# Kernel optimization log

Measured on AMD Instinct MI355X. Metric: run time of the kernel, lower is better.

The kernel has to match this reference:

```python
import jax, jax.numpy as jnp
import numpy as np

N = 262144
H = 256
R = 32


def setup_inputs() -> dict:
    key = jax.random.key(0)
    ks = jax.random.split(key, 16)
    s = 1.0 / np.sqrt(H)
    return {
        "x": jax.random.normal(ks[0], (N, 1), jnp.float32),
        "t": jax.random.uniform(ks[1], (N, 1), jnp.float32),
        "start_w": jax.random.normal(ks[2], (H, 2), jnp.float32) * 0.5,
        "start_b": jax.random.normal(ks[3], (H,), jnp.float32) * 0.1,
        "end_w": jax.random.normal(ks[4], (1, H), jnp.float32) * s,
        "end_b": jax.random.normal(ks[5], (1,), jnp.float32) * 0.1,
        "col_0": jax.random.normal(ks[6], (H, R), jnp.float32) * s,
        "col_1": jax.random.normal(ks[7], (H, R), jnp.float32) * s,
        "col_2": jax.random.normal(ks[8], (H, R), jnp.float32) * s,
        "row_0": jax.random.normal(ks[9], (H, R), jnp.float32) * s,
        "row_1": jax.random.normal(ks[10], (H, R), jnp.float32) * s,
        "row_2": jax.random.normal(ks[11], (H, R), jnp.float32) * s,
        "alpha_0": jax.random.normal(ks[12], (R,), jnp.float32),
        "alpha_1": jax.random.normal(ks[13], (R,), jnp.float32),
        "alpha_2": jax.random.normal(ks[14], (R,), jnp.float32),
    }


def reference(x, t, start_w, start_b, end_w, end_b,
              col_0, col_1, col_2, row_0, row_1, row_2,
              alpha_0, alpha_1, alpha_2):
    # inputs: [N,2] -> start Linear -> tanh
    inp = jnp.concatenate([x, t], axis=1)
    h = jnp.tanh(inp @ start_w.T + start_b)  # [N, H]
    # three low-rank blocks: h @ (col * diag(alpha)) @ row.T, then tanh.
    # col_basis @ diag(alpha) == col_basis * alpha[None, :] (column scaling)
    for col, row, alpha in ((col_0, row_0, alpha_0),
                            (col_1, row_1, alpha_1),
                            (col_2, row_2, alpha_2)):
        h = jnp.tanh((h @ (col * alpha)) @ row.T)  # [N,H]->[N,R]->[N,H]
    return h @ end_w.T + end_b  # [N, 1]
```

## Files before the change

kernel.cpp:

```cpp
#include <hip/hip_runtime.h>


typedef _Float16 half4_t __attribute__((ext_vector_type(4)));
typedef float    float4_t __attribute__((ext_vector_type(4)));

namespace {

struct Smem {
  half4_t ctf[3 * 16 * 2 * 64];
  half4_t rwf[3 * 16 * 2 * 64];
  float w0[256], w1[256], bb[256], ew[256];
};

__device__ __forceinline__ float fast_tanh(float x) {
  float e = __builtin_amdgcn_exp2f(x * 2.885390081777927f);
  return 1.0f - 2.0f * __builtin_amdgcn_rcpf(e + 1.0f);
}

__device__ __forceinline__ half4_t tanh4_pack(float4_t v) {
  half4_t h;
  h.x = (_Float16)fast_tanh(v.x);
  h.y = (_Float16)fast_tanh(v.y);
  h.z = (_Float16)fast_tanh(v.z);
  h.w = (_Float16)fast_tanh(v.w);
  return h;
}

__device__ __forceinline__ half4_t pack16(float4_t v) {
  half4_t h;
  h.x = (_Float16)v.x; h.y = (_Float16)v.y; h.z = (_Float16)v.z; h.w = (_Float16)v.w;
  return h;
}

__global__ __launch_bounds__(1024)
__attribute__((amdgpu_waves_per_eu(4, 4)))
void pinn_fused(
    const float* __restrict__ xg, const float* __restrict__ tg,
    const float* __restrict__ sw, const float* __restrict__ sb,
    const float* __restrict__ ewp, const float* __restrict__ ebp,
    const float* __restrict__ c0, const float* __restrict__ c1,
    const float* __restrict__ c2, const float* __restrict__ r0,
    const float* __restrict__ r1, const float* __restrict__ r2,
    const float* __restrict__ a0, const float* __restrict__ a1,
    const float* __restrict__ a2, float* __restrict__ out, int n)
{
  __shared__ Smem sm;
  const int tid = threadIdx.x;

  for (int e = tid; e < 3 * 16 * 2 * 64; e += 1024) {
    const int lane_ = e & 63;
    const int sel   = (e >> 6) & 1;
    const int t_    = (e >> 7) & 15;
    const int k_    = e >> 11;
    const int m_ = lane_ & 15, q_ = lane_ >> 4;
    const float* ck = (k_ == 0) ? c0 : (k_ == 1) ? c1 : c2;
    const float* rk = (k_ == 0) ? r0 : (k_ == 1) ? r1 : r2;
    const float* ak = (k_ == 0) ? a0 : (k_ == 1) ? a1 : a2;
    {
      const int r = sel * 16 + m_;
      const float av = ak[r];
      const int j0 = 16 * t_ + 4 * q_;
      half4_t v;
      v.x = (_Float16)(ck[(j0 + 0) * 32 + r] * av);
      v.y = (_Float16)(ck[(j0 + 1) * 32 + r] * av);
      v.z = (_Float16)(ck[(j0 + 2) * 32 + r] * av);
      v.w = (_Float16)(ck[(j0 + 3) * 32 + r] * av);
      sm.ctf[e] = v;
    }
    {
      const int j = 16 * t_ + m_;
      const int rr = sel * 16 + 4 * q_;
      half4_t v;
      v.x = (_Float16)rk[j * 32 + rr + 0];
      v.y = (_Float16)rk[j * 32 + rr + 1];
      v.z = (_Float16)rk[j * 32 + rr + 2];
      v.w = (_Float16)rk[j * 32 + rr + 3];
      sm.rwf[e] = v;
    }
  }
  if (tid < 256) {
    sm.w0[tid] = sw[2 * tid];
    sm.w1[tid] = sw[2 * tid + 1];
    sm.bb[tid] = sb[tid];
    sm.ew[tid] = ewp[tid];
  }
  __syncthreads();

  const int wave = tid >> 6;
  const int lane = tid & 63;
  const int m = lane & 15;
  const int q = lane >> 4;
  const int wo = 4 * q;
  const float ebv = ebp[0];
  const int tiles = n >> 4;

#pragma unroll 1
  for (int g = blockIdx.x * 32 + wave * 2; g < tiles; g += 8192) {
    const int n0 = g * 16;
    const int n1 = n0 + 16;
    const float xm0 = xg[n0 + m], tm0 = tg[n0 + m];
    const float xm1 = xg[n1 + m], tm1 = tg[n1 + m];

    float4_t a00 = {0.f, 0.f, 0.f, 0.f}, a01 = {0.f, 0.f, 0.f, 0.f};
    float4_t a10 = {0.f, 0.f, 0.f, 0.f}, a11 = {0.f, 0.f, 0.f, 0.f};
#pragma unroll 1
    for (int t = 0; t < 16; ++t) {
      const int cb = t * 16 + wo;
      const float4_t w0v = *(const float4_t*)&sm.w0[cb];
      const float4_t w1v = *(const float4_t*)&sm.w1[cb];
      const float4_t bv  = *(const float4_t*)&sm.bb[cb];
      float4_t z0, z1;
      z0.x = fmaf(xm0, w0v.x, fmaf(tm0, w1v.x, bv.x));
      z0.y = fmaf(xm0, w0v.y, fmaf(tm0, w1v.y, bv.y));
      z0.z = fmaf(xm0, w0v.z, fmaf(tm0, w1v.z, bv.z));
      z0.w = fmaf(xm0, w0v.w, fmaf(tm0, w1v.w, bv.w));
      z1.x = fmaf(xm1, w0v.x, fmaf(tm1, w1v.x, bv.x));
      z1.y = fmaf(xm1, w0v.y, fmaf(tm1, w1v.y, bv.y));
      z1.z = fmaf(xm1, w0v.z, fmaf(tm1, w1v.z, bv.z));
      z1.w = fmaf(xm1, w0v.w, fmaf(tm1, w1v.w, bv.w));
      const half4_t h0 = tanh4_pack(z0);
      const half4_t h1 = tanh4_pack(z1);
      const half4_t cA = sm.ctf[t * 128 + lane];
      const half4_t cB = sm.ctf[t * 128 + 64 + lane];
      a00 = __builtin_amdgcn_mfma_f32_16x16x16f16(cA, h0, a00, 0, 0, 0);
      a01 = __builtin_amdgcn_mfma_f32_16x16x16f16(cB, h0, a01, 0, 0, 0);
      a10 = __builtin_amdgcn_mfma_f32_16x16x16f16(cA, h1, a10, 0, 0, 0);
      a11 = __builtin_amdgcn_mfma_f32_16x16x16f16(cB, h1, a11, 0, 0, 0);
    }

    float ssum0 = 0.0f, ssum1 = 0.0f;
#pragma unroll 1
    for (int k = 0; k < 3; ++k) {
      const half4_t pA0 = pack16(a00), pB0 = pack16(a01);
      const half4_t pA1 = pack16(a10), pB1 = pack16(a11);

      if (k < 2) {
        float4_t n00 = {0.f, 0.f, 0.f, 0.f}, n01 = {0.f, 0.f, 0.f, 0.f};
        float4_t n10 = {0.f, 0.f, 0.f, 0.f}, n11 = {0.f, 0.f, 0.f, 0.f};
        const half4_t* rp = &sm.rwf[k * 2048 + lane];
        const half4_t* cp = &sm.ctf[(k + 1) * 2048 + lane];
#pragma unroll 1
        for (int t = 0; t < 16; ++t) {
          const half4_t rA = rp[0], rB = rp[64];
          const half4_t cA = cp[0], cB = cp[64];
          float4_t hc0 = {0.f, 0.f, 0.f, 0.f};
          hc0 = __builtin_amdgcn_mfma_f32_16x16x16f16(rA, pA0, hc0, 0, 0, 0);
          hc0 = __builtin_amdgcn_mfma_f32_16x16x16f16(rB, pB0, hc0, 0, 0, 0);
          float4_t hc1 = {0.f, 0.f, 0.f, 0.f};
          hc1 = __builtin_amdgcn_mfma_f32_16x16x16f16(rA, pA1, hc1, 0, 0, 0);
          hc1 = __builtin_amdgcn_mfma_f32_16x16x16f16(rB, pB1, hc1, 0, 0, 0);
          const half4_t h0 = tanh4_pack(hc0);
          const half4_t h1 = tanh4_pack(hc1);
          n00 = __builtin_amdgcn_mfma_f32_16x16x16f16(cA, h0, n00, 0, 0, 0);
          n01 = __builtin_amdgcn_mfma_f32_16x16x16f16(cB, h0, n01, 0, 0, 0);
          n10 = __builtin_amdgcn_mfma_f32_16x16x16f16(cA, h1, n10, 0, 0, 0);
          n11 = __builtin_amdgcn_mfma_f32_16x16x16f16(cB, h1, n11, 0, 0, 0);
          rp += 128;
          cp += 128;
        }
        a00 = n00; a01 = n01; a10 = n10; a11 = n11;
      } else {
        const half4_t* rp = &sm.rwf[2 * 2048 + lane];
#pragma unroll 1
        for (int t = 0; t < 16; ++t) {
          const half4_t rA = rp[0], rB = rp[64];
          float4_t hc0 = {0.f, 0.f, 0.f, 0.f};
          hc0 = __builtin_amdgcn_mfma_f32_16x16x16f16(rA, pA0, hc0, 0, 0, 0);
          hc0 = __builtin_amdgcn_mfma_f32_16x16x16f16(rB, pB0, hc0, 0, 0, 0);
          float4_t hc1 = {0.f, 0.f, 0.f, 0.f};
          hc1 = __builtin_amdgcn_mfma_f32_16x16x16f16(rA, pA1, hc1, 0, 0, 0);
          hc1 = __builtin_amdgcn_mfma_f32_16x16x16f16(rB, pB1, hc1, 0, 0, 0);
          const float4_t ev = *(const float4_t*)&sm.ew[t * 16 + wo];
          ssum0 += fast_tanh(hc0.x) * ev.x + fast_tanh(hc0.y) * ev.y
                 + fast_tanh(hc0.z) * ev.z + fast_tanh(hc0.w) * ev.w;
          ssum1 += fast_tanh(hc1.x) * ev.x + fast_tanh(hc1.y) * ev.y
                 + fast_tanh(hc1.z) * ev.z + fast_tanh(hc1.w) * ev.w;
          rp += 128;
        }
      }
    }
    ssum0 += __shfl_xor(ssum0, 16);
    ssum0 += __shfl_xor(ssum0, 32);
    ssum1 += __shfl_xor(ssum1, 16);
    ssum1 += __shfl_xor(ssum1, 32);
    if (lane < 16) {
      out[n0 + m] = ssum0 + ebv;
      out[n1 + m] = ssum1 + ebv;
    }
  }
}

}

extern "C" void kernel_launch(void* const* d_in, const int* in_sizes, int n_in,
                              void* d_out, int out_size, void* d_ws, size_t ws_size,
                              hipStream_t stream) {
  const float* xg  = (const float*)d_in[0];
  const float* tg  = (const float*)d_in[1];
  const float* sw  = (const float*)d_in[2];
  const float* sb  = (const float*)d_in[3];
  const float* ewp = (const float*)d_in[4];
  const float* ebp = (const float*)d_in[5];
  const float* c0  = (const float*)d_in[6];
  const float* c1  = (const float*)d_in[7];
  const float* c2  = (const float*)d_in[8];
  const float* r0  = (const float*)d_in[9];
  const float* r1  = (const float*)d_in[10];
  const float* r2  = (const float*)d_in[11];
  const float* a0  = (const float*)d_in[12];
  const float* a1  = (const float*)d_in[13];
  const float* a2  = (const float*)d_in[14];
  float* outp = (float*)d_out;

  const int n = in_sizes[0];

  pinn_fused<<<256, 1024, 0, stream>>>(xg, tg, sw, sb, ewp, ebp,
                                       c0, c1, c2, r0, r1, r2, a0, a1, a2,
                                       outp, n);
}
```

Baseline: 153.8 us.

## Fold tanh affine parts into weights and batch reciprocals across eight values

After: 160.2 us. 4.1% more time.

```diff
diff --git a/kernel.cpp b/kernel.cpp
--- a/kernel.cpp
+++ b/kernel.cpp
@@ -4,26 +4,37 @@
 typedef _Float16 half4_t __attribute__((ext_vector_type(4)));
 typedef float    float4_t __attribute__((ext_vector_type(4)));
 
+#define TANH_SCALE 2.885390081777927f
+#define ECLAMP 32768.0f
+
 namespace {
 
-struct Smem {
+struct alignas(16) Smem {
   half4_t ctf[3 * 16 * 2 * 64];
   half4_t rwf[3 * 16 * 2 * 64];
-  float w0[256], w1[256], bb[256], ew[256];
+  float w0[256], w1[256], bb[256];
+  float ew[256];
+  float rsC[3 * 32];
 };
 
-__device__ __forceinline__ float fast_tanh(float x) {
-  float e = __builtin_amdgcn_exp2f(x * 2.885390081777927f);
-  return 1.0f - 2.0f * __builtin_amdgcn_rcpf(e + 1.0f);
-}
-
-__device__ __forceinline__ half4_t tanh4_pack(float4_t v) {
-  half4_t h;
-  h.x = (_Float16)fast_tanh(v.x);
-  h.y = (_Float16)fast_tanh(v.y);
-  h.z = (_Float16)fast_tanh(v.z);
-  h.w = (_Float16)fast_tanh(v.w);
-  return h;
+__device__ __forceinline__ void inv8(float4_t v0, float4_t v1,
+                                     float4_t& i0, float4_t& i1) {
+  const float a0 = fminf(__builtin_amdgcn_exp2f(v0.x), ECLAMP) + 1.0f;
+  const float a1 = fminf(__builtin_amdgcn_exp2f(v0.y), ECLAMP) + 1.0f;
+  const float a2 = fminf(__builtin_amdgcn_exp2f(v0.z), ECLAMP) + 1.0f;
+  const float a3 = fminf(__builtin_amdgcn_exp2f(v0.w), ECLAMP) + 1.0f;
+  const float a4 = fminf(__builtin_amdgcn_exp2f(v1.x), ECLAMP) + 1.0f;
+  const float a5 = fminf(__builtin_amdgcn_exp2f(v1.y), ECLAMP) + 1.0f;
+  const float a6 = fminf(__builtin_amdgcn_exp2f(v1.z), ECLAMP) + 1.0f;
+  const float a7 = fminf(__builtin_amdgcn_exp2f(v1.w), ECLAMP) + 1.0f;
+  const float p01 = a0 * a1, p23 = a2 * a3, p45 = a4 * a5, p67 = a6 * a7;
+  const float q03 = p01 * p23, q47 = p45 * p67;
+  const float rd = __builtin_amdgcn_rcpf(q03 * q47);
+  const float s03 = rd * q47, s47 = rd * q03;
+  const float t01 = s03 * p23, t23 = s03 * p01;
+  const float t45 = s47 * p67, t67 = s47 * p45;
+  i0.x = t01 * a1; i0.y = t01 * a0; i0.z = t23 * a3; i0.w = t23 * a2;
+  i1.x = t45 * a5; i1.y = t45 * a4; i1.z = t67 * a7; i1.w = t67 * a6;
 }
 
 __device__ __forceinline__ half4_t pack16(float4_t v) {
@@ -58,7 +69,7 @@
     const float* ak = (k_ == 0) ? a0 : (k_ == 1) ? a1 : a2;
     {
       const int r = sel * 16 + m_;
-      const float av = ak[r];
+      const float av = ak[r] * -2.0f;
       const int j0 = 16 * t_ + 4 * q_;
       half4_t v;
       v.x = (_Float16)(ck[(j0 + 0) * 32 + r] * av);
@@ -71,18 +82,31 @@
       const int j = 16 * t_ + m_;
       const int rr = sel * 16 + 4 * q_;
       half4_t v;
-      v.x = (_Float16)rk[j * 32 + rr + 0];
-      v.y = (_Float16)rk[j * 32 + rr + 1];
-      v.z = (_Float16)rk[j * 32 + rr + 2];
-      v.w = (_Float16)rk[j * 32 + rr + 3];
+      v.x = (_Float16)(rk[j * 32 + rr + 0] * TANH_SCALE);
+      v.y = (_Float16)(rk[j * 32 + rr + 1] * TANH_SCALE);
+      v.z = (_Float16)(rk[j * 32 + rr + 2] * TANH_SCALE);
+      v.w = (_Float16)(rk[j * 32 + rr + 3] * TANH_SCALE);
       sm.rwf[e] = v;
     }
   }
   if (tid < 256) {
-    sm.w0[tid] = sw[2 * tid];
-    sm.w1[tid] = sw[2 * tid + 1];
-    sm.bb[tid] = sb[tid];
-    sm.ew[tid] = ewp[tid];
+    sm.w0[tid] = sw[2 * tid] * TANH_SCALE;
+    sm.w1[tid] = sw[2 * tid + 1] * TANH_SCALE;
+    sm.bb[tid] = sb[tid] * TANH_SCALE;
+    sm.ew[tid] = ewp[tid] * -2.0f;
+  }
+  __syncthreads();
+
+  if (tid < 96) {
+    const int k_ = tid >> 5, r = tid & 31;
+    const int sel = r >> 4, mm = r & 15;
+    float s = 0.0f;
+    for (int t = 0; t < 16; ++t)
+      for (int qq = 0; qq < 4; ++qq) {
+        const half4_t v = sm.ctf[((k_ * 16 + t) * 2 + sel) * 64 + 16 * qq + mm];
+        s += (float)v.x + (float)v.y + (float)v.z + (float)v.w;
+      }
+    sm.rsC[k_ * 32 + r] = -0.5f * s;
   }
   __syncthreads();
 
@@ -94,6 +118,13 @@
   const float ebv = ebp[0];
   const int tiles = n >> 4;
 
+  float ewsum = 0.0f;
+  for (int t = 0; t < 16; ++t) {
+    const float4_t e4 = *(const float4_t*)&sm.ew[t * 16 + wo];
+    ewsum += e4.x + e4.y + e4.z + e4.w;
+  }
+  ewsum *= -0.5f;
+
 #pragma unroll 1
   for (int g = blockIdx.x * 32 + wave * 2; g < tiles; g += 8192) {
     const int n0 = g * 16;
@@ -101,8 +132,10 @@
     const float xm0 = xg[n0 + m], tm0 = tg[n0 + m];
     const float xm1 = xg[n1 + m], tm1 = tg[n1 + m];
 
-    float4_t a00 = {0.f, 0.f, 0.f, 0.f}, a01 = {0.f, 0.f, 0.f, 0.f};
-    float4_t a10 = {0.f, 0.f, 0.f, 0.f}, a11 = {0.f, 0.f, 0.f, 0.f};
+    const float4_t rs00 = *(const float4_t*)&sm.rsC[0 * 32 + wo];
+    const float4_t rs01 = *(const float4_t*)&sm.rsC[0 * 32 + 16 + wo];
+    float4_t a00 = rs00, a01 = rs01;
+    float4_t a10 = rs00, a11 = rs01;
 #pragma unroll 1
     for (int t = 0; t < 16; ++t) {
       const int cb = t * 16 + wo;
@@ -111,32 +144,35 @@
       const float4_t bv  = *(const float4_t*)&sm.bb[cb];
       float4_t z0, z1;
       z0.x = fmaf(xm0, w0v.x, fmaf(tm0, w1v.x, bv.x));
+      z1.x = fmaf(xm1, w0v.x, fmaf(tm1, w1v.x, bv.x));
       z0.y = fmaf(xm0, w0v.y, fmaf(tm0, w1v.y, bv.y));
+      z1.y = fmaf(xm1, w0v.y, fmaf(tm1, w1v.y, bv.y));
       z0.z = fmaf(xm0, w0v.z, fmaf(tm0, w1v.z, bv.z));
+      z1.z = fmaf(xm1, w0v.z, fmaf(tm1, w1v.z, bv.z));
       z0.w = fmaf(xm0, w0v.w, fmaf(tm0, w1v.w, bv.w));
-      z1.x = fmaf(xm1, w0v.x, fmaf(tm1, w1v.x, bv.x));
-      z1.y = fmaf(xm1, w0v.y, fmaf(tm1, w1v.y, bv.y));
-      z1.z = fmaf(xm1, w0v.z, fmaf(tm1, w1v.z, bv.z));
       z1.w = fmaf(xm1, w0v.w, fmaf(tm1, w1v.w, bv.w));
-      const half4_t h0 = tanh4_pack(z0);
-      const half4_t h1 = tanh4_pack(z1);
+      float4_t i0, i1;
+      inv8(z0, z1, i0, i1);
+      const half4_t h0 = pack16(i0);
+      const half4_t h1 = pack16(i1);
       const half4_t cA = sm.ctf[t * 128 + lane];
       const half4_t cB = sm.ctf[t * 128 + 64 + lane];
       a00 = __builtin_amdgcn_mfma_f32_16x16x16f16(cA, h0, a00, 0, 0, 0);
+      a10 = __builtin_amdgcn_mfma_f32_16x16x16f16(cA, h1, a10, 0, 0, 0);
       a01 = __builtin_amdgcn_mfma_f32_16x16x16f16(cB, h0, a01, 0, 0, 0);
-      a10 = __builtin_amdgcn_mfma_f32_16x16x16f16(cA, h1, a10, 0, 0, 0);
       a11 = __builtin_amdgcn_mfma_f32_16x16x16f16(cB, h1, a11, 0, 0, 0);
     }
 
-    float ssum0 = 0.0f, ssum1 = 0.0f;
+    float ssum0 = ewsum, ssum1 = ewsum;
 #pragma unroll 1
     for (int k = 0; k < 3; ++k) {
       const half4_t pA0 = pack16(a00), pB0 = pack16(a01);
       const half4_t pA1 = pack16(a10), pB1 = pack16(a11);
 
       if (k < 2) {
-        float4_t n00 = {0.f, 0.f, 0.f, 0.f}, n01 = {0.f, 0.f, 0.f, 0.f};
-        float4_t n10 = {0.f, 0.f, 0.f, 0.f}, n11 = {0.f, 0.f, 0.f, 0.f};
+        const float4_t rsA = *(const float4_t*)&sm.rsC[(k + 1) * 32 + wo];
+        const float4_t rsB = *(const float4_t*)&sm.rsC[(k + 1) * 32 + 16 + wo];
+        float4_t n00 = rsA, n01 = rsB, n10 = rsA, n11 = rsB;
         const half4_t* rp = &sm.rwf[k * 2048 + lane];
         const half4_t* cp = &sm.ctf[(k + 1) * 2048 + lane];
 #pragma unroll 1
@@ -144,16 +180,18 @@
           const half4_t rA = rp[0], rB = rp[64];
           const half4_t cA = cp[0], cB = cp[64];
           float4_t hc0 = {0.f, 0.f, 0.f, 0.f};
+          float4_t hc1 = {0.f, 0.f, 0.f, 0.f};
           hc0 = __builtin_amdgcn_mfma_f32_16x16x16f16(rA, pA0, hc0, 0, 0, 0);
+          hc1 = __builtin_amdgcn_mfma_f32_16x16x16f16(rA, pA1, hc1, 0, 0, 0);
           hc0 = __builtin_amdgcn_mfma_f32_16x16x16f16(rB, pB0, hc0, 0, 0, 0);
-          float4_t hc1 = {0.f, 0.f, 0.f, 0.f};
-          hc1 = __builtin_amdgcn_mfma_f32_16x16x16f16(rA, pA1, hc1, 0, 0, 0);
           hc1 = __builtin_amdgcn_mfma_f32_16x16x16f16(rB, pB1, hc1, 0, 0, 0);
-          const half4_t h0 = tanh4_pack(hc0);
-          const half4_t h1 = tanh4_pack(hc1);
+          float4_t i0, i1;
+          inv8(hc0, hc1, i0, i1);
+          const half4_t h0 = pack16(i0);
+          const half4_t h1 = pack16(i1);
           n00 = __builtin_amdgcn_mfma_f32_16x16x16f16(cA, h0, n00, 0, 0, 0);
+          n10 = __builtin_amdgcn_mfma_f32_16x16x16f16(cA, h1, n10, 0, 0, 0);
           n01 = __builtin_amdgcn_mfma_f32_16x16x16f16(cB, h0, n01, 0, 0, 0);
-          n10 = __builtin_amdgcn_mfma_f32_16x16x16f16(cA, h1, n10, 0, 0, 0);
           n11 = __builtin_amdgcn_mfma_f32_16x16x16f16(cB, h1, n11, 0, 0, 0);
           rp += 128;
           cp += 128;
@@ -165,16 +203,16 @@
         for (int t = 0; t < 16; ++t) {
           const half4_t rA = rp[0], rB = rp[64];
           float4_t hc0 = {0.f, 0.f, 0.f, 0.f};
+          float4_t hc1 = {0.f, 0.f, 0.f, 0.f};
           hc0 = __builtin_amdgcn_mfma_f32_16x16x16f16(rA, pA0, hc0, 0, 0, 0);
+          hc1 = __builtin_amdgcn_mfma_f32_16x16x16f16(rA, pA1, hc1, 0, 0, 0);
           hc0 = __builtin_amdgcn_mfma_f32_16x16x16f16(rB, pB0, hc0, 0, 0, 0);
-          float4_t hc1 = {0.f, 0.f, 0.f, 0.f};
-          hc1 = __builtin_amdgcn_mfma_f32_16x16x16f16(rA, pA1, hc1, 0, 0, 0);
           hc1 = __builtin_amdgcn_mfma_f32_16x16x16f16(rB, pB1, hc1, 0, 0, 0);
+          float4_t i0, i1;
+          inv8(hc0, hc1, i0, i1);
           const float4_t ev = *(const float4_t*)&sm.ew[t * 16 + wo];
-          ssum0 += fast_tanh(hc0.x) * ev.x + fast_tanh(hc0.y) * ev.y
-                 + fast_tanh(hc0.z) * ev.z + fast_tanh(hc0.w) * ev.w;
-          ssum1 += fast_tanh(hc1.x) * ev.x + fast_tanh(hc1.y) * ev.y
-                 + fast_tanh(hc1.z) * ev.z + fast_tanh(hc1.w) * ev.w;
+          ssum0 += ev.x * i0.x + ev.y * i0.y + ev.z * i0.z + ev.w * i0.w;
+          ssum1 += ev.x * i1.x + ev.y * i1.y + ev.z * i1.z + ev.w * i1.w;
           rp += 128;
         }
       }
```

## Software-pipeline MFMA/tanh loops and fold tanh scale into weights

Applied to the files above, without the earlier changes.

Result: faster. 150.1 us (-2.4%).

```diff
diff --git a/kernel.cpp b/kernel.cpp
--- a/kernel.cpp
+++ b/kernel.cpp
@@ -2,34 +2,39 @@
 
 
 typedef _Float16 half4_t __attribute__((ext_vector_type(4)));
+typedef _Float16 half2_t __attribute__((ext_vector_type(2)));
+typedef __fp16   fp16x2  __attribute__((ext_vector_type(2)));
 typedef float    float4_t __attribute__((ext_vector_type(4)));
 
+#define TANH_SCALE 2.885390081777927f
+#define MFMA16 __builtin_amdgcn_mfma_f32_16x16x16f16
+
 namespace {
 
-struct Smem {
+struct alignas(16) Smem {
   half4_t ctf[3 * 16 * 2 * 64];
   half4_t rwf[3 * 16 * 2 * 64];
-  float w0[256], w1[256], bb[256], ew[256];
+  float w0[256], w1[256], bb[256];
+  float ew[256];
 };
 
-__device__ __forceinline__ float fast_tanh(float x) {
-  float e = __builtin_amdgcn_exp2f(x * 2.885390081777927f);
-  return 1.0f - 2.0f * __builtin_amdgcn_rcpf(e + 1.0f);
-}
-
-__device__ __forceinline__ half4_t tanh4_pack(float4_t v) {
-  half4_t h;
-  h.x = (_Float16)fast_tanh(v.x);
-  h.y = (_Float16)fast_tanh(v.y);
-  h.z = (_Float16)fast_tanh(v.z);
-  h.w = (_Float16)fast_tanh(v.w);
-  return h;
-}
-
-__device__ __forceinline__ half4_t pack16(float4_t v) {
-  half4_t h;
-  h.x = (_Float16)v.x; h.y = (_Float16)v.y; h.z = (_Float16)v.z; h.w = (_Float16)v.w;
-  return h;
+__device__ __forceinline__ half4_t pack4(float4_t v) {
+  union { fp16x2 f2[2]; half4_t h4; } u;
+  u.f2[0] = __builtin_amdgcn_cvt_pkrtz(v.x, v.y);
+  u.f2[1] = __builtin_amdgcn_cvt_pkrtz(v.z, v.w);
+  return u.h4;
+}
+
+__device__ __forceinline__ float tanh_pre(float y) {
+  const float e = __builtin_amdgcn_exp2f(y);
+  return fmaf(-2.0f, __builtin_amdgcn_rcpf(e + 1.0f), 1.0f);
+}
+
+__device__ __forceinline__ half4_t tanh4(float4_t v) {
+  float4_t r;
+  r.x = tanh_pre(v.x); r.y = tanh_pre(v.y);
+  r.z = tanh_pre(v.z); r.w = tanh_pre(v.w);
+  return pack4(r);
 }
 
 __global__ __launch_bounds__(1024)
@@ -71,17 +76,17 @@
       const int j = 16 * t_ + m_;
       const int rr = sel * 16 + 4 * q_;
       half4_t v;
-      v.x = (_Float16)rk[j * 32 + rr + 0];
-      v.y = (_Float16)rk[j * 32 + rr + 1];
-      v.z = (_Float16)rk[j * 32 + rr + 2];
-      v.w = (_Float16)rk[j * 32 + rr + 3];
+      v.x = (_Float16)(rk[j * 32 + rr + 0] * TANH_SCALE);
+      v.y = (_Float16)(rk[j * 32 + rr + 1] * TANH_SCALE);
+      v.z = (_Float16)(rk[j * 32 + rr + 2] * TANH_SCALE);
+      v.w = (_Float16)(rk[j * 32 + rr + 3] * TANH_SCALE);
       sm.rwf[e] = v;
     }
   }
   if (tid < 256) {
-    sm.w0[tid] = sw[2 * tid];
-    sm.w1[tid] = sw[2 * tid + 1];
-    sm.bb[tid] = sb[tid];
+    sm.w0[tid] = sw[2 * tid] * TANH_SCALE;
+    sm.w1[tid] = sw[2 * tid + 1] * TANH_SCALE;
+    sm.bb[tid] = sb[tid] * TANH_SCALE;
     sm.ew[tid] = ewp[tid];
   }
   __syncthreads();
@@ -94,6 +99,8 @@
   const float ebv = ebp[0];
   const int tiles = n >> 4;
 
+  const float4_t z4 = {0.f, 0.f, 0.f, 0.f};
+
 #pragma unroll 1
   for (int g = blockIdx.x * 32 + wave * 2; g < tiles; g += 8192) {
     const int n0 = g * 16;
@@ -101,84 +108,146 @@
     const float xm0 = xg[n0 + m], tm0 = tg[n0 + m];
     const float xm1 = xg[n1 + m], tm1 = tg[n1 + m];
 
-    float4_t a00 = {0.f, 0.f, 0.f, 0.f}, a01 = {0.f, 0.f, 0.f, 0.f};
-    float4_t a10 = {0.f, 0.f, 0.f, 0.f}, a11 = {0.f, 0.f, 0.f, 0.f};
-#pragma unroll 1
-    for (int t = 0; t < 16; ++t) {
-      const int cb = t * 16 + wo;
+    float4_t a00 = z4, a01 = z4, a10 = z4, a11 = z4;
+    float4_t zc0, zc1;
+    {
+      const float4_t w0v = *(const float4_t*)&sm.w0[wo];
+      const float4_t w1v = *(const float4_t*)&sm.w1[wo];
+      const float4_t bv  = *(const float4_t*)&sm.bb[wo];
+      zc0.x = fmaf(xm0, w0v.x, fmaf(tm0, w1v.x, bv.x));
+      zc1.x = fmaf(xm1, w0v.x, fmaf(tm1, w1v.x, bv.x));
+      zc0.y = fmaf(xm0, w0v.y, fmaf(tm0, w1v.y, bv.y));
+      zc1.y = fmaf(xm1, w0v.y, fmaf(tm1, w1v.y, bv.y));
+      zc0.z = fmaf(xm0, w0v.z, fmaf(tm0, w1v.z, bv.z));
+      zc1.z = fmaf(xm1, w0v.z, fmaf(tm1, w1v.z, bv.z));
+      zc0.w = fmaf(xm0, w0v.w, fmaf(tm0, w1v.w, bv.w));
+      zc1.w = fmaf(xm1, w0v.w, fmaf(tm1, w1v.w, bv.w));
+    }
+    const half4_t* cp0 = &sm.ctf[lane];
+#pragma unroll 1
+    for (int t = 0; t < 15; ++t) {
+      const int cb = (t + 1) * 16 + wo;
       const float4_t w0v = *(const float4_t*)&sm.w0[cb];
       const float4_t w1v = *(const float4_t*)&sm.w1[cb];
       const float4_t bv  = *(const float4_t*)&sm.bb[cb];
-      float4_t z0, z1;
-      z0.x = fmaf(xm0, w0v.x, fmaf(tm0, w1v.x, bv.x));
-      z0.y = fmaf(xm0, w0v.y, fmaf(tm0, w1v.y, bv.y));
-      z0.z = fmaf(xm0, w0v.z, fmaf(tm0, w1v.z, bv.z));
-      z0.w = fmaf(xm0, w0v.w, fmaf(tm0, w1v.w, bv.w));
-      z1.x = fmaf(xm1, w0v.x, fmaf(tm1, w1v.x, bv.x));
-      z1.y = fmaf(xm1, w0v.y, fmaf(tm1, w1v.y, bv.y));
-      z1.z = fmaf(xm1, w0v.z, fmaf(tm1, w1v.z, bv.z));
-      z1.w = fmaf(xm1, w0v.w, fmaf(tm1, w1v.w, bv.w));
-      const half4_t h0 = tanh4_pack(z0);
-      const half4_t h1 = tanh4_pack(z1);
-      const half4_t cA = sm.ctf[t * 128 + lane];
-      const half4_t cB = sm.ctf[t * 128 + 64 + lane];
-      a00 = __builtin_amdgcn_mfma_f32_16x16x16f16(cA, h0, a00, 0, 0, 0);
-      a01 = __builtin_amdgcn_mfma_f32_16x16x16f16(cB, h0, a01, 0, 0, 0);
-      a10 = __builtin_amdgcn_mfma_f32_16x16x16f16(cA, h1, a10, 0, 0, 0);
-      a11 = __builtin_amdgcn_mfma_f32_16x16x16f16(cB, h1, a11, 0, 0, 0);
+      const half4_t h0 = tanh4(zc0);
+      const half4_t h1 = tanh4(zc1);
+      float4_t zn0, zn1;
+      zn0.x = fmaf(xm0, w0v.x, fmaf(tm0, w1v.x, bv.x));
+      zn1.x = fmaf(xm1, w0v.x, fmaf(tm1, w1v.x, bv.x));
+      zn0.y = fmaf(xm0, w0v.y, fmaf(tm0, w1v.y, bv.y));
+      zn1.y = fmaf(xm1, w0v.y, fmaf(tm1, w1v.y, bv.y));
+      zn0.z = fmaf(xm0, w0v.z, fmaf(tm0, w1v.z, bv.z));
+      zn1.z = fmaf(xm1, w0v.z, fmaf(tm1, w1v.z, bv.z));
+      zn0.w = fmaf(xm0, w0v.w, fmaf(tm0, w1v.w, bv.w));
+      zn1.w = fmaf(xm1, w0v.w, fmaf(tm1, w1v.w, bv.w));
+      const half4_t cA = cp0[0], cB = cp0[64];
+      a00 = MFMA16(cA, h0, a00, 0, 0, 0);
+      a10 = MFMA16(cA, h1, a10, 0, 0, 0);
+      a01 = MFMA16(cB, h0, a01, 0, 0, 0);
+      a11 = MFMA16(cB, h1, a11, 0, 0, 0);
+      zc0 = zn0; zc1 = zn1;
+      cp0 += 128;
+    }
+    {
+      const half4_t h0 = tanh4(zc0);
+      const half4_t h1 = tanh4(zc1);
+      const half4_t cA = cp0[0], cB = cp0[64];
+      a00 = MFMA16(cA, h0, a00, 0, 0, 0);
+      a10 = MFMA16(cA, h1, a10, 0, 0, 0);
+      a01 = MFMA16(cB, h0, a01, 0, 0, 0);
+      a11 = MFMA16(cB, h1, a11, 0, 0, 0);
+    }
+
+#pragma unroll 1
+    for (int k = 0; k < 2; ++k) {
+      const half4_t pA0 = pack4(a00), pB0 = pack4(a01);
+      const half4_t pA1 = pack4(a10), pB1 = pack4(a11);
+      const half4_t* rp = &sm.rwf[k * 2048 + lane];
+      const half4_t* cp = &sm.ctf[(k + 1) * 2048 + lane];
+      float4_t hc0, hc1;
+      {
+        const half4_t rA = rp[0], rB = rp[64];
+        hc0 = MFMA16(rA, pA0, z4, 0, 0, 0);
+        hc1 = MFMA16(rA, pA1, z4, 0, 0, 0);
+        hc0 = MFMA16(rB, pB0, hc0, 0, 0, 0);
+        hc1 = MFMA16(rB, pB1, hc1, 0, 0, 0);
+      }
+      float4_t n00 = z4, n01 = z4, n10 = z4, n11 = z4;
+#pragma unroll 1
+      for (int t = 0; t < 15; ++t) {
+        const half4_t rA = rp[128], rB = rp[192];
+        const half4_t cA = cp[0],  cB = cp[64];
+        const half4_t h0 = tanh4(hc0);
+        const half4_t h1 = tanh4(hc1);
+        float4_t u0 = MFMA16(rA, pA0, z4, 0, 0, 0);
+        float4_t u1 = MFMA16(rA, pA1, z4, 0, 0, 0);
+        u0 = MFMA16(rB, pB0, u0, 0, 0, 0);
+        u1 = MFMA16(rB, pB1, u1, 0, 0, 0);
+        n00 = MFMA16(cA, h0, n00, 0, 0, 0);
+        n10 = MFMA16(cA, h1, n10, 0, 0, 0);
+        n01 = MFMA16(cB, h0, n01, 0, 0, 0);
+        n11 = MFMA16(cB, h1, n11, 0, 0, 0);
+        hc0 = u0; hc1 = u1;
+        rp += 128; cp += 128;
+      }
+      {
+        const half4_t cA = cp[0], cB = cp[64];
+        const half4_t h0 = tanh4(hc0);
+        const half4_t h1 = tanh4(hc1);
+        n00 = MFMA16(cA, h0, n00, 0, 0, 0);
+        n10 = MFMA16(cA, h1, n10, 0, 0, 0);
+        n01 = MFMA16(cB, h0, n01, 0, 0, 0);
+        n11 = MFMA16(cB, h1, n11, 0, 0, 0);
+      }
+      a00 = n00; a01 = n01; a10 = n10; a11 = n11;
     }
 
     float ssum0 = 0.0f, ssum1 = 0.0f;
-#pragma unroll 1
-    for (int k = 0; k < 3; ++k) {
-      const half4_t pA0 = pack16(a00), pB0 = pack16(a01);
-      const half4_t pA1 = pack16(a10), pB1 = pack16(a11);
-
-      if (k < 2) {
-        float4_t n00 = {0.f, 0.f, 0.f, 0.f}, n01 = {0.f, 0.f, 0.f, 0.f};
-        float4_t n10 = {0.f, 0.f, 0.f, 0.f}, n11 = {0.f, 0.f, 0.f, 0.f};
-        const half4_t* rp = &sm.rwf[k * 2048 + lane];
-        const half4_t* cp = &sm.ctf[(k + 1) * 2048 + lane];
-#pragma unroll 1
-        for (int t = 0; t < 16; ++t) {
-          const half4_t rA = rp[0], rB = rp[64];
-          const half4_t cA = cp[0], cB = cp[64];
-          float4_t hc0 = {0.f, 0.f, 0.f, 0.f};
-          hc0 = __builtin_amdgcn_mfma_f32_16x16x16f16(rA, pA0, hc0, 0, 0, 0);
-          hc0 = __builtin_amdgcn_mfma_f32_16x16x16f16(rB, pB0, hc0, 0, 0, 0);
-          float4_t hc1 = {0.f, 0.f, 0.f, 0.f};
-          hc1 = __builtin_amdgcn_mfma_f32_16x16x16f16(rA, pA1, hc1, 0, 0, 0);
-          hc1 = __builtin_amdgcn_mfma_f32_16x16x16f16(rB, pB1, hc1, 0, 0, 0);
-          const half4_t h0 = tanh4_pack(hc0);
-          const half4_t h1 = tanh4_pack(hc1);
-          n00 = __builtin_amdgcn_mfma_f32_16x16x16f16(cA, h0, n00, 0, 0, 0);
-          n01 = __builtin_amdgcn_mfma_f32_16x16x16f16(cB, h0, n01, 0, 0, 0);
-          n10 = __builtin_amdgcn_mfma_f32_16x16x16f16(cA, h1, n10, 0, 0, 0);
-          n11 = __builtin_amdgcn_mfma_f32_16x16x16f16(cB, h1, n11, 0, 0, 0);
-          rp += 128;
-          cp += 128;
-        }
-        a00 = n00; a01 = n01; a10 = n10; a11 = n11;
-      } else {
-        const half4_t* rp = &sm.rwf[2 * 2048 + lane];
-#pragma unroll 1
-        for (int t = 0; t < 16; ++t) {
-          const half4_t rA = rp[0], rB = rp[64];
-          float4_t hc0 = {0.f, 0.f, 0.f, 0.f};
-          hc0 = __builtin_amdgcn_mfma_f32_16x16x16f16(rA, pA0, hc0, 0, 0, 0);
-          hc0 = __builtin_amdgcn_mfma_f32_16x16x16f16(rB, pB0, hc0, 0, 0, 0);
-          float4_t hc1 = {0.f, 0.f, 0.f, 0.f};
-          hc1 = __builtin_amdgcn_mfma_f32_16x16x16f16(rA, pA1, hc1, 0, 0, 0);
-          hc1 = __builtin_amdgcn_mfma_f32_16x16x16f16(rB, pB1, hc1, 0, 0, 0);
-          const float4_t ev = *(const float4_t*)&sm.ew[t * 16 + wo];
-          ssum0 += fast_tanh(hc0.x) * ev.x + fast_tanh(hc0.y) * ev.y
-                 + fast_tanh(hc0.z) * ev.z + fast_tanh(hc0.w) * ev.w;
-          ssum1 += fast_tanh(hc1.x) * ev.x + fast_tanh(hc1.y) * ev.y
-                 + fast_tanh(hc1.z) * ev.z + fast_tanh(hc1.w) * ev.w;
-          rp += 128;
-        }
-      }
-    }
+    {
+      const half4_t pA0 = pack4(a00), pB0 = pack4(a01);
+      const half4_t pA1 = pack4(a10), pB1 = pack4(a11);
+      const half4_t* rp = &sm.rwf[2 * 2048 + lane];
+      float4_t hc0, hc1;
+      {
+        const half4_t rA = rp[0], rB = rp[64];
+        hc0 = MFMA16(rA, pA0, z4, 0, 0, 0);
+        hc1 = MFMA16(rA, pA1, z4, 0, 0, 0);
+        hc0 = MFMA16(rB, pB0, hc0, 0, 0, 0);
+        hc1 = MFMA16(rB, pB1, hc1, 0, 0, 0);
+      }
+#pragma unroll 1
+      for (int t = 0; t < 15; ++t) {
+        const half4_t rA = rp[128], rB = rp[192];
+        const float4_t ev = *(const float4_t*)&sm.ew[t * 16 + wo];
+        float4_t u0 = MFMA16(rA, pA0, z4, 0, 0, 0);
+        float4_t u1 = MFMA16(rA, pA1, z4, 0, 0, 0);
+        u0 = MFMA16(rB, pB0, u0, 0, 0, 0);
+        u1 = MFMA16(rB, pB1, u1, 0, 0, 0);
+        ssum0 = fmaf(ev.x, tanh_pre(hc0.x), ssum0);
+        ssum1 = fmaf(ev.x, tanh_pre(hc1.x), ssum1);
+        ssum0 = fmaf(ev.y, tanh_pre(hc0.y), ssum0);
+        ssum1 = fmaf(ev.y, tanh_pre(hc1.y), ssum1);
+        ssum0 = fmaf(ev.z, tanh_pre(hc0.z), ssum0);
+        ssum1 = fmaf(ev.z, tanh_pre(hc1.z), ssum1);
+        ssum0 = fmaf(ev.w, tanh_pre(hc0.w), ssum0);
+        ssum1 = fmaf(ev.w, tanh_pre(hc1.w), ssum1);
+        hc0 = u0; hc1 = u1;
+        rp += 128;
+      }
+      {
+        const float4_t ev = *(const float4_t*)&sm.ew[240 + wo];
+        ssum0 = fmaf(ev.x, tanh_pre(hc0.x), ssum0);
+        ssum1 = fmaf(ev.x, tanh_pre(hc1.x), ssum1);
+        ssum0 = fmaf(ev.y, tanh_pre(hc0.y), ssum0);
+        ssum1 = fmaf(ev.y, tanh_pre(hc1.y), ssum1);
+        ssum0 = fmaf(ev.z, tanh_pre(hc0.z), ssum0);
+        ssum1 = fmaf(ev.z, tanh_pre(hc1.z), ssum1);
+        ssum0 = fmaf(ev.w, tanh_pre(hc0.w), ssum0);
+        ssum1 = fmaf(ev.w, tanh_pre(hc1.w), ssum1);
+      }
+    }
+
     ssum0 += __shfl_xor(ssum0, 16);
     ssum0 += __shfl_xor(ssum0, 32);
     ssum1 += __shfl_xor(ssum1, 16);
```
